# Performance work log

Measured on AMD Instinct MI355X. Metric: run time of the kernel, lower is better.

Reference implementation:

```python
import jax, jax.numpy as jnp
import numpy as np
import math

MUL = 16                      # num_in_features == num_out_features
LDIMS = (1, 3, 5)             # 0e, 1o, 2e  (lmax = 2)
FEAT = MUL * sum(LDIMS)       # 144 = irreps dim = number_of_basis
PATHS = [(0,0,0),(1,1,0),(2,2,0),
         (0,1,1),(1,0,1),(1,2,1),(2,1,1),
         (0,2,2),(1,1,2),(2,0,2),(2,2,2)]
DOT_PATHS = [(0,0,0),(1,1,0),(2,2,0)]

# ---------- real Wigner-3j / Clebsch-Gordan (e3nn convention), numpy precompute ----------

def _su2_cg(j1, m1, j2, m2, j3, m3):
    if m3 != m1 + m2:
        return 0.0
    f = math.factorial
    vmin = max(-j1 + j2 + m3, -j1 + m1, 0)
    vmax = min(j2 + j3 + m1, j3 - j1 + j2, j3 + m3)
    C = math.sqrt((2*j3+1) * f(j3+j1-j2) * f(j3-j1+j2) * f(j1+j2-j3)
                  * f(j3+m3) * f(j3-m3)
                  / (f(j1+j2+j3+1) * f(j1-m1) * f(j1+m1) * f(j2-m2) * f(j2+m2)))
    S = 0.0
    for v in range(vmin, vmax + 1):
        S += (-1.0)**(v + j2 + m2) * f(j2+j3+m1-v) * f(j1-m1+v) / (
            f(v) * f(j3-j1+j2-v) * f(j3+m3-v) * f(v+j1-j2-m3))
    return C * S

def _qmat(l):
    # complex -> real spherical-harmonic change of basis (e3nn convention)
    q = np.zeros((2*l+1, 2*l+1), dtype=np.complex128)
    for m in range(-l, 0):
        q[l+m, l+abs(m)] = 1.0/math.sqrt(2)
        q[l+m, l-abs(m)] = -1j/math.sqrt(2)
    q[l, l] = 1.0
    for m in range(1, l+1):
        q[l+m, l+abs(m)] = (-1)**m/math.sqrt(2)
        q[l+m, l-abs(m)] = 1j*(-1)**m/math.sqrt(2)
    return (-1j)**l * q

def _real_w3j(l1, l2, l3):
    C = np.zeros((2*l1+1, 2*l2+1, 2*l3+1))
    for i, m1 in enumerate(range(-l1, l1+1)):
        for j, m2 in enumerate(range(-l2, l2+1)):
            for k, m3 in enumerate(range(-l3, l3+1)):
                C[i, j, k] = _su2_cg(l1, m1, l2, m2, l3, m3)
    Cr = np.einsum('ij,kl,mn,ikn->jlm', _qmat(l1), _qmat(l2),
                   np.conj(_qmat(l3).T), C.astype(np.complex128))
    Cr = np.real(Cr)
    return (Cr / np.linalg.norm(Cr)).astype(np.float32)  # unit Frobenius norm (3j convention)

W3J = {p: _real_w3j(*p) for p in set(PATHS)}

# ---------- fully connected tensor product (component/element normalization) ----------

def _split(x):
    # blocked layout: [mul x 0e | mul x 1o | mul x 2e]
    n = x.shape[0]
    xs, o = [], 0
    for d in LDIMS:
        xs.append(x[:, o:o + MUL*d].reshape(n, MUL, d))
        o += MUL * d
    return xs

def _fctp(x1, x2, W):
    # W: [11, u, v, w] stacked per PATHS
    xs1, xs2 = _split(x1), _split(x2)
    n = x1.shape[0]
    n_paths = {l3: sum(1 for p in PATHS if p[2] == l3) for l3 in range(3)}
    outs = [None, None, None]
    for i, (l1, l2, l3) in enumerate(PATHS):
        C = jnp.asarray(W3J[(l1, l2, l3)])          # [i, j, k]
        scale = math.sqrt((2*l3 + 1) / (n_paths[l3] * MUL * MUL))
        a = jnp.einsum('nvj,ijk->nivk', xs2[l2], C)      # [n, i, v, k]
        b = jnp.einsum('nui,nivk->nuvk', xs1[l1], a)     # [n, u, v, k]
        o = scale * jnp.einsum('nuvk,uvw->nwk', b, W[i]) # [n, w, k]
        outs[l3] = o if outs[l3] is None else outs[l3] + o
    return jnp.concatenate([o.reshape(n, -1) for o in outs], axis=1)  # [n, 9*MUL]

def _dot(x1, x2, Wd):
    # FCTP(irreps_input, irreps_input, '0e'): paths (0,0,0),(1,1,0),(2,2,0), out mul = 1
    xs1, xs2 = _split(x1), _split(x2)
    fan = 3 * MUL * MUL
    acc = 0.0
    for i, (l1, l2, l3) in enumerate(DOT_PATHS):
        C = jnp.asarray(W3J[(l1, l2, l3)])[:, :, 0]      # [i, j]
        t = jnp.einsum('nui,ij,nvj->nuv', xs1[l1], C, xs2[l2])
        acc = acc + jnp.einsum('nuv,uv->n', t, Wd[i])
    return (acc * math.sqrt(1.0 / fan))[:, None]         # [n, 1]

def setup_inputs() -> dict:
    key = jax.random.key(0)
    ks = jax.random.split(key, 8)
    N = 50000
    return {
        'nodes_features': jax.random.normal(ks[0], (N, FEAT), jnp.float32),
        'degree_matrix': jax.random.normal(ks[1], (N,), jnp.float32),
        'edges_features_distance': jax.random.normal(ks[2], (N,), jnp.float32),
        'edges_features_bond': jax.random.normal(ks[3], (N,), jnp.float32),
        'w_q': jax.random.normal(ks[4], (11, MUL, MUL, MUL), jnp.float32),
        'w_k': jax.random.normal(ks[5], (11, MUL, MUL, MUL), jnp.float32),
        'w_v': jax.random.normal(ks[6], (11, MUL, MUL, MUL), jnp.float32),
        'w_dot': jax.random.normal(ks[7], (3, MUL, MUL), jnp.float32),
    }

def reference(nodes_features, degree_matrix, edges_features_distance,
              edges_features_bond, w_q, w_k, w_v, w_dot):
    # degree_matrix / edges_features_* are unused by the original forward
    x = nodes_features
    q = _fctp(x, x, w_q)                   # tp_q(x, x)
    k = _fctp(x, x, w_k)                   # tp_k(x, x)
    v = _fctp(x, x, w_v)                   # tp(x, x)
    d = _dot(q, k, w_dot)                  # [n, 1]
    e = jnp.exp(d / math.sqrt(float(FEAT)))
    attn = e / (e + 1e-10)                 # sum over last dim of size 1 + eps
    out = attn * v                         # dropout is identity in eval mode
    out = out.reshape(-1, MUL)             # view(-1, num_heads * num_out_features)
    return jax.nn.elu(out)                 # [9n, MUL]
```

## Files before the change

### kernel.cpp

```cpp
#include <hip/hip_runtime.h>
#include <math.h>

#define NP 11
#define NN 8

__device__ __constant__ int g_l1[NP]   = {0,1,2,0,1,1,2,0,1,2,2};
__device__ __constant__ int g_l2[NP]   = {0,1,2,1,0,2,1,2,1,0,2};
__device__ __constant__ int g_l3[NP]   = {0,0,0,1,1,1,1,2,2,2,2};
__device__ __constant__ int g_coff[NP] = {0,1,10,35,44,53,98,143,168,213,238};

typedef _Float16 half8 __attribute__((ext_vector_type(8)));
typedef _Float16 h2 __attribute__((ext_vector_type(2)));
typedef float f32x4 __attribute__((ext_vector_type(4)));

__device__ __forceinline__ float bfu(unsigned int v){ return __uint_as_float(v<<16); }
__device__ __forceinline__ unsigned int rne16(float f){
  unsigned int ui=__float_as_uint(f);
  return (ui+0x7fffu+((ui>>16)&1u))>>16;
}
__device__ __forceinline__ unsigned short h16(float f){
  _Float16 h=(_Float16)f;
  return __builtin_bit_cast(unsigned short,h);
}

__device__ double dfact(int n){ double r=1.0; for(int i=2;i<=n;++i) r*=(double)i; return r; }

__device__ double su2_cg(int j1,int m1,int j2,int m2,int j3,int m3){
  if(m1+m2!=m3) return 0.0;
  int vmin=-j1+j2+m3; if(-j1+m1>vmin) vmin=-j1+m1; if(vmin<0) vmin=0;
  int vmax=j2+j3+m1; int t=j3-j1+j2; if(t<vmax) vmax=t; t=j3+m3; if(t<vmax) vmax=t;
  double C = sqrt((double)(2*j3+1)*dfact(j3+j1-j2)*dfact(j3-j1+j2)*dfact(j1+j2-j3)
      *dfact(j3+m3)*dfact(j3-m3)
      /(dfact(j1+j2+j3+1)*dfact(j1-m1)*dfact(j1+m1)*dfact(j2-m2)*dfact(j2+m2)));
  double S=0.0;
  for(int v=vmin;v<=vmax;++v){
    double sg = ((v+j2+m2)&1)? -1.0:1.0;
    S += sg*dfact(j2+j3+m1-v)*dfact(j1-m1+v)
        /(dfact(v)*dfact(j3-j1+j2-v)*dfact(j3+m3-v)*dfact(v+j1-j2-m3));
  }
  return C*S;
}

__device__ void qelem(int l,int r,int c,double &re,double &im){
  int m=r-l; double a=0.0,b=0.0; const double s=0.70710678118654752440;
  if(m<0){ if(c==l-m) a=s; else if(c==l+m) b=-s; }
  else if(m==0){ if(c==l) a=1.0; }
  else { double sg=(m&1)?-1.0:1.0; if(c==l+m) a=sg*s; else if(c==l-m) b=sg*s; }
  if(l==1){ double tt=a; a=b; b=-tt; }
  else if(l==2){ a=-a; b=-b; }
  re=a; im=b;
}

__device__ int probe_f32(const unsigned short* __restrict__ p, int nelem, int* scnt){
  if(threadIdx.x==0) *scnt=0;
  __syncthreads();
  int M = nelem < 4096 ? nelem : 4096;
  int c=0;
  for(int t=threadIdx.x;t<M;t+=blockDim.x){
    unsigned e=((unsigned)p[t]>>7)&0xFFu;
    if(e!=0u && (e<0x70u || e>0x8Eu)) ++c;
  }
  atomicAdd(scnt,c);
  __syncthreads();
  return (*scnt*8 > M) ? 1 : 0;
}

__global__ void prep(const unsigned short* __restrict__ x,
                     const unsigned short* __restrict__ wq,
                     const unsigned short* __restrict__ wk,
                     const unsigned short* __restrict__ wv,
                     const unsigned short* __restrict__ wd,
                     int nx,int nw,int nd,
                     float* __restrict__ c3j, unsigned int* __restrict__ cgh,
                     unsigned int* __restrict__ wpre){
  const int p=blockIdx.x, tp=blockIdx.y;
  __shared__ double cg[125];
  __shared__ double outv[125];
  __shared__ double nrm;
  __shared__ int scnt;

  const unsigned short* ww=(tp==0)?wq:((tp==1)?wk:wv);
  const int f32 = probe_f32(ww,nw,&scnt);

  {
    unsigned int* dst=wpre+(size_t)(p*3+tp)*2240;
    for(int t=threadIdx.x;t<2048;t+=256){
      int w=t>>7, c=t&127;
      int i0=c*32+w, i1=i0+16;
      float f0,f1;
      if(f32){
        const float* wf=(const float*)ww+(size_t)p*4096;
        f0=wf[i0]; f1=wf[i1];
      }else{
        const unsigned short* wsp=ww+(size_t)p*4096;
        f0=bfu(wsp[i0]); f1=bfu(wsp[i1]);
      }
      dst[w*140+c]=(unsigned int)h16(f0)|((unsigned int)h16(f1)<<16);
    }
  }

  if(tp==0){
    int l1=g_l1[p], l2=g_l2[p], l3=g_l3[p];
    int d1=2*l1+1, d2=2*l2+1, d3=2*l3+1;
    int tot=d1*d2*d3;
    for(int t=threadIdx.x;t<tot;t+=256){
      int i=t/(d2*d3), k=(t/d3)%d2, n=t%d3;
      cg[t]=su2_cg(l1,i-l1,l2,k-l2,l3,n-l3);
    }
    __syncthreads();
    for(int t=threadIdx.x;t<tot;t+=256){
      int a=t/(d2*d3), b=(t/d3)%d2, c=t%d3;
      double sre=0.0;
      for(int i=0;i<d1;++i){ double q1r,q1i; qelem(l1,i,a,q1r,q1i);
        for(int k=0;k<d2;++k){ double q2r,q2i; qelem(l2,k,b,q2r,q2i);
          double pr=q1r*q2r-q1i*q2i, pi=q1r*q2i+q1i*q2r;
          for(int n=0;n<d3;++n){ double q3r,q3i; qelem(l3,n,c,q3r,q3i);
            sre += (pr*q3r + pi*q3i) * cg[(i*d2+k)*d3+n];
          }
        }
      }
      outv[t]=sre;
    }
    __syncthreads();
    if(threadIdx.x==0){
      double s=0.0; for(int t=0;t<tot;++t) s+=outv[t]*outv[t];
      nrm=sqrt(s);
    }
    __syncthreads();
    const float scl_[3]={0.03608439182435161f,0.05412658773652741f,0.06987712429686843f};
    float s=scl_[l3];
    for(int t=threadIdx.x;t<tot;t+=256){
      float val=(float)(outv[t]/nrm);
      c3j[g_coff[p]+t]=val;
      unsigned int h=(unsigned int)h16(val*s);
      cgh[g_coff[p]+t]=h|(h<<16);
    }
  }

  if(p==0 && tp==0){
    int xf=probe_f32(x,nx,&scnt);
    if(threadIdx.x==0) c3j[363]=(float)xf;
    int df=probe_f32(wd,nd,&scnt);
    if(threadIdx.x==0) c3j[367]=(float)df;
  }
}

template<int D1,int D2,int D3>
__device__ __forceinline__ void fusedAB(const unsigned int* __restrict__ sXp,
                                        const unsigned int* __restrict__ sXd,
                                        const unsigned int* __restrict__ cgp,
                                        unsigned int* __restrict__ sAu,
                                        int wave, int lane, int nvalid){
  constexpr int O1=(D1==1)?0:((D1==3)?16:64);
  constexpr int O2P=(D2==1)?0:((D2==3)?8:32);
  const int nn=lane>>3, vp=lane&7;
  if(nn>=nvalid) return;
  h2 x2p[D2];
  #pragma unroll
  for(int j=0;j<D2;++j) x2p[j]=__builtin_bit_cast(h2,sXp[nn*76+O2P+vp*D2+j]);
  const int u0=wave*2;
  h2 x1a[D1],x1b[D1];
  #pragma unroll
  for(int i=0;i<D1;++i){
    x1a[i]=__builtin_bit_cast(h2,sXd[nn*148+O1+u0*D1+i]);
    x1b[i]=__builtin_bit_cast(h2,sXd[nn*148+O1+(u0+1)*D1+i]);
  }
  h2 acc0[D3],acc1[D3];
  #pragma unroll
  for(int k=0;k<D3;++k){ acc0[k]=(h2){(_Float16)0.f,(_Float16)0.f}; acc1[k]=acc0[k]; }
  #pragma unroll
  for(int i=0;i<D1;++i){
    #pragma unroll
    for(int k=0;k<D3;++k){
      h2 ar=(h2){(_Float16)0.f,(_Float16)0.f};
      #pragma unroll
      for(int j=0;j<D2;++j)
        ar+=__builtin_bit_cast(h2,cgp[(i*D2+j)*D3+k])*x2p[j];
      acc0[k]+=x1a[i]*ar;
      acc1[k]+=x1b[i]*ar;
    }
  }
  #pragma unroll
  for(int k=0;k<D3;++k){
    sAu[(k*8+nn)*140+u0*8+vp]   =__builtin_bit_cast(unsigned int,acc0[k]);
    sAu[(k*8+nn)*140+u0*8+vp+8] =__builtin_bit_cast(unsigned int,acc1[k]);
  }
}

template<int L3>
__device__ __forceinline__ void stage2_acc(const unsigned int* __restrict__ sAu,
                                           const unsigned int* __restrict__ wp_path,
                                           const uint4* __restrict__ bf,
                                           f32x4& a0, f32x4& a1,
                                           int n16, int quad, int wave){
  constexpr int P=(L3+1)*3;
  if(wave<P){
    int Mt=wave/3;
    const unsigned int* ap=sAu+(Mt*16+n16)*140+quad*4;
    f32x4 a=a0;
    #pragma unroll
    for(int ks=0;ks<8;++ks)
      a=__builtin_amdgcn_mfma_f32_16x16x32_f16(
          *reinterpret_cast<const half8*>(ap+ks*16),
          __builtin_bit_cast(half8,bf[ks]),a,0,0,0);
    a0=a;
  }
  if(L3==2 && wave==0){
    const unsigned int* ap=sAu+(2*16+n16)*140+quad*4;
    const uint4* bp=(const uint4*)(wp_path+2*2240+n16*140+quad*4);
    uint4 b2[8];
    #pragma unroll
    for(int ks=0;ks<8;++ks) b2[ks]=bp[ks*4];
    f32x4 a=a1;
    #pragma unroll
    for(int ks=0;ks<8;++ks)
      a=__builtin_amdgcn_mfma_f32_16x16x32_f16(
          *reinterpret_cast<const half8*>(ap+ks*16),
          __builtin_bit_cast(half8,b2[ks]),a,0,0,0);
    a1=a;
  }
}

template<int L3>
__device__ __forceinline__ void stage2_out(const f32x4& a0, const f32x4& a1,
                                           float* __restrict__ sO,
                                           int n16, int quad, int wave){
  constexpr int D3=2*L3+1;
  constexpr int OO=(L3==0)?0:((L3==1)?16:64);
  constexpr int P=(L3+1)*3;
  if(wave<P){
    int tp=wave%3, Mt=wave/3;
    #pragma unroll
    for(int reg=0;reg<4;++reg){
      int row=Mt*16+quad*4+reg;
      int k=row>>3, node=row&7;
      if(k<D3) sO[node*440+tp*144+OO+n16*D3+k]=a0[reg];
    }
  }
  if(L3==2 && wave==0){
    #pragma unroll
    for(int reg=0;reg<4;++reg){
      int row=32+quad*4+reg;
      int k=row>>3, node=row&7;
      if(k<D3) sO[node*440+2*144+OO+n16*D3+k]=a1[reg];
    }
  }
}

__global__ __launch_bounds__(512,6) void tfn_main(
    const unsigned short* __restrict__ xin,
    const unsigned int* __restrict__ wpre,
    const unsigned int* __restrict__ cgh,
    const unsigned short* __restrict__ wd,
    const float* __restrict__ c3j,
    unsigned short* __restrict__ outp, int N)
{
  __shared__ __align__(16) unsigned int sAu[48*140];
  __shared__ float sO[NN*440];
  __shared__ __align__(8) unsigned int sXp[NN*76];
  __shared__ __align__(8) unsigned int sXd[NN*148];
  __shared__ float sWd[768];

  const int tid=threadIdx.x;
  const int wave=tid>>6, lane=tid&63;
  const int n16=lane&15, quad=lane>>4;
  const int node0=blockIdx.x*NN;
  const int nvalid=(N-node0)<NN?(N-node0):NN;

  const int xf32 = c3j[363]!=0.0f;
  const int df32 = c3j[367]!=0.0f;

  float* scratch=sO;
  if(!xf32){
    for(int t=tid;t<NN*36;t+=512){
      int nn=t/36, w4=t%36;
      if(nn<nvalid){
        uint2 u=((const uint2*)(xin+(size_t)(node0+nn)*144))[w4];
        float* dst=&scratch[nn*144+w4*4];
        dst[0]=bfu(u.x&0xffffu); dst[1]=bfu(u.x>>16);
        dst[2]=bfu(u.y&0xffffu); dst[3]=bfu(u.y>>16);
      }
    }
  }else{
    const float* xf=(const float*)xin;
    for(int t=tid;t<NN*144;t+=512){
      int nn=t/144, f=t%144;
      if(nn<nvalid) scratch[nn*144+f]=xf[(size_t)(node0+nn)*144+f];
    }
  }
  if(!df32){ for(int t=tid;t<768;t+=512) sWd[t]=bfu((unsigned int)wd[t]); }
  else     { const float* wdf=(const float*)wd; for(int t=tid;t<768;t+=512) sWd[t]=wdf[t]; }
  __syncthreads();

  for(int t=tid;t<NN*144;t+=512){
    int nn=t/144, f=t-nn*144;
    unsigned int h=(unsigned int)h16(scratch[t]);
    sXd[nn*148+f]=h|(h<<16);
  }
  for(int t=tid;t<NN*72;t+=512){
    int nn=t/72, g=t-nn*72;
    int fa,fb;
    if(g<8){ fa=2*g; fb=fa+1; }
    else if(g<32){ int gg=g-8; int vp=gg/3, j=gg-3*vp; fa=16+(2*vp)*3+j; fb=fa+3; }
    else { int gg=g-32; int vp=gg/5, j=gg-5*vp; fa=64+(2*vp)*5+j; fb=fa+5; }
    sXp[nn*76+g]=(unsigned int)h16(scratch[nn*144+fa])|((unsigned int)h16(scratch[nn*144+fb])<<16);
  }
  __syncthreads();

  #define PATH_STEP(P_,D1_,D2_,D3_) { \
    const int PT=((D3_-1)/2+1)*3; \
    uint4 bf[8]; \
    if(wave<PT){ \
      const uint4* bp=(const uint4*)(wpre+(size_t)P_*6720+(wave%3)*2240+n16*140+quad*4); \
      bf[0]=bp[0];  bf[1]=bp[4];  bf[2]=bp[8];  bf[3]=bp[12]; \
      bf[4]=bp[16]; bf[5]=bp[20]; bf[6]=bp[24]; bf[7]=bp[28]; \
    } \
    fusedAB<D1_,D2_,D3_>(sXp,sXd,cgh+g_coff[P_],sAu,wave,lane,nvalid); \
    __syncthreads(); \
    stage2_acc<(D3_-1)/2>(sAu,wpre+(size_t)P_*6720,bf,a0,a1,n16,quad,wave); \
    __syncthreads(); }

  {
    f32x4 a0={0.f,0.f,0.f,0.f}, a1={0.f,0.f,0.f,0.f};
    PATH_STEP(0,1,1,1)
    PATH_STEP(1,3,3,1)
    PATH_STEP(2,5,5,1)
    stage2_out<0>(a0,a1,sO,n16,quad,wave);
  }
  {
    f32x4 a0={0.f,0.f,0.f,0.f}, a1={0.f,0.f,0.f,0.f};
    PATH_STEP(3,1,3,3)
    PATH_STEP(4,3,1,3)
    PATH_STEP(5,3,5,3)
    PATH_STEP(6,5,3,3)
    stage2_out<1>(a0,a1,sO,n16,quad,wave);
  }
  {
    f32x4 a0={0.f,0.f,0.f,0.f}, a1={0.f,0.f,0.f,0.f};
    PATH_STEP(7,1,5,5)
    PATH_STEP(8,3,3,5)
    PATH_STEP(9,5,1,5)
    PATH_STEP(10,5,5,5)
    stage2_out<2>(a0,a1,sO,n16,quad,wave);
  }
  #undef PATH_STEP
  __syncthreads();

  {
    int node=wave;
    if(node<nvalid){
      const float c0=c3j[0], c1=c3j[1], c2=c3j[10];
      const float* qv=sO+node*440;
      const float* kv=qv+144;
      const int v=lane&15, ug=lane>>4;
      float k0=kv[v];
      float k1[3],k2[5];
      #pragma unroll
      for(int j=0;j<3;++j) k1[j]=kv[16+v*3+j];
      #pragma unroll
      for(int m=0;m<5;++m) k2[m]=kv[64+v*5+m];
      float part=0.f;
      #pragma unroll
      for(int t=0;t<4;++t){
        int u=ug+4*t;
        float d0=qv[u]*k0;
        float d1=0.f;
        #pragma unroll
        for(int j=0;j<3;++j) d1+=qv[16+u*3+j]*k1[j];
        float d2=0.f;
        #pragma unroll
        for(int m=0;m<5;++m) d2+=qv[64+u*5+m]*k2[m];
        part+=sWd[u*16+v]*(c0*d0)+sWd[256+u*16+v]*(c1*d1)+sWd[512+u*16+v]*(c2*d2);
      }
      #pragma unroll
      for(int off=1;off<64;off<<=1) part+=__shfl_xor(part,off,64);
      float dd=part*0.03608439182435161f;
      float ex=dd*(1.0f/12.0f);
      ex=fminf(fmaxf(ex,-80.f),80.f);
      float e=expf(ex);
      float attn=e/(e+1e-10f);
      const float* vv=sO+node*440+288;
      if(!xf32){
        unsigned short* ob=outp+(size_t)(node0+node)*144;
        for(int f=lane;f<144;f+=64){
          float val=attn*vv[f];
          float r=(val>0.f)?val:expm1f(val);
          ob[f]=(unsigned short)rne16(r);
        }
      }else{
        float* ob=(float*)outp+(size_t)(node0+node)*144;
        for(int f=lane;f<144;f+=64){
          float val=attn*vv[f];
          ob[f]=(val>0.f)?val:expm1f(val);
        }
      }
    }
  }
}

extern "C" void kernel_launch(void* const* d_in, const int* in_sizes, int n_in,
                              void* d_out, int out_size, void* d_ws, size_t ws_size,
                              hipStream_t stream){
  (void)n_in; (void)out_size; (void)ws_size;
  const unsigned short* x =(const unsigned short*)d_in[0];
  const unsigned short* wq=(const unsigned short*)d_in[4];
  const unsigned short* wk=(const unsigned short*)d_in[5];
  const unsigned short* wv=(const unsigned short*)d_in[6];
  const unsigned short* wd=(const unsigned short*)d_in[7];
  float* c3j=(float*)d_ws;
  unsigned int* cgh=(unsigned int*)d_ws+1024;
  unsigned int* wpre=(unsigned int*)d_ws+2048;
  int N=in_sizes[0]/144;
  prep<<<dim3(NP,3),dim3(256),0,stream>>>(x,wq,wk,wv,wd,
      in_sizes[0],in_sizes[4],in_sizes[7],c3j,cgh,wpre);
  int nb=(N+NN-1)/NN;
  tfn_main<<<dim3(nb),dim3(512),0,stream>>>(x,wpre,cgh,wd,c3j,(unsigned short*)d_out,N);
}
```

Before: 354.9 us.

## Pack LDS into one buffer, store outputs in fp16, cache CG in LDS

Merges all shared arrays into a single overlapping LDS buffer. The q/k/v outputs and the dot weights are now stored as fp16 instead of fp32, and the CG coefficients are staged in LDS instead of read from global memory. The smaller LDS footprint lets launch bounds go from 6 to 8 blocks per CU, which is meant to raise occupancy. The cost is lower precision in the q·k dot product and the v values, plus tighter register limits.

New measurement: 565.9 us. 59.5% more time.

```diff
diff --git a/kernel.cpp b/kernel.cpp
--- a/kernel.cpp
+++ b/kernel.cpp
@@ -21,6 +21,9 @@
 __device__ __forceinline__ unsigned short h16(float f){
   _Float16 h=(_Float16)f;
   return __builtin_bit_cast(unsigned short,h);
+}
+__device__ __forceinline__ float hf(unsigned short s){
+  return (float)__builtin_bit_cast(_Float16,s);
 }
 
 __device__ double dfact(int n){ double r=1.0; for(int i=2;i<=n;++i) r*=(double)i; return r; }
@@ -145,9 +148,16 @@
   }
 }
 
+#define L_AU   0
+#define L_SO   5600
+#define L_XP   7392
+#define L_XD   8000
+#define L_WD   9184
+#define L_CG   9568
+#define L_TOT  9932
+
 template<int D1,int D2,int D3>
-__device__ __forceinline__ void fusedAB(const unsigned int* __restrict__ sXp,
-                                        const unsigned int* __restrict__ sXd,
+__device__ __forceinline__ void fusedAB(const unsigned int* __restrict__ lds,
                                         const unsigned int* __restrict__ cgp,
                                         unsigned int* __restrict__ sAu,
                                         int wave, int lane, int nvalid){
@@ -157,13 +167,13 @@
   if(nn>=nvalid) return;
   h2 x2p[D2];
   #pragma unroll
-  for(int j=0;j<D2;++j) x2p[j]=__builtin_bit_cast(h2,sXp[nn*76+O2P+vp*D2+j]);
+  for(int j=0;j<D2;++j) x2p[j]=__builtin_bit_cast(h2,lds[L_XP+nn*76+O2P+vp*D2+j]);
   const int u0=wave*2;
   h2 x1a[D1],x1b[D1];
   #pragma unroll
   for(int i=0;i<D1;++i){
-    x1a[i]=__builtin_bit_cast(h2,sXd[nn*148+O1+u0*D1+i]);
-    x1b[i]=__builtin_bit_cast(h2,sXd[nn*148+O1+(u0+1)*D1+i]);
+    x1a[i]=__builtin_bit_cast(h2,lds[L_XD+nn*148+O1+u0*D1+i]);
+    x1b[i]=__builtin_bit_cast(h2,lds[L_XD+nn*148+O1+(u0+1)*D1+i]);
   }
   h2 acc0[D3],acc1[D3];
   #pragma unroll
@@ -223,7 +233,7 @@
 
 template<int L3>
 __device__ __forceinline__ void stage2_out(const f32x4& a0, const f32x4& a1,
-                                           float* __restrict__ sO,
+                                           unsigned short* __restrict__ sOh,
                                            int n16, int quad, int wave){
   constexpr int D3=2*L3+1;
   constexpr int OO=(L3==0)?0:((L3==1)?16:64);
@@ -234,7 +244,7 @@
     for(int reg=0;reg<4;++reg){
       int row=Mt*16+quad*4+reg;
       int k=row>>3, node=row&7;
-      if(k<D3) sO[node*440+tp*144+OO+n16*D3+k]=a0[reg];
+      if(k<D3) sOh[node*448+tp*144+OO+n16*D3+k]=h16(a0[reg]);
     }
   }
   if(L3==2 && wave==0){
@@ -242,12 +252,12 @@
     for(int reg=0;reg<4;++reg){
       int row=32+quad*4+reg;
       int k=row>>3, node=row&7;
-      if(k<D3) sO[node*440+2*144+OO+n16*D3+k]=a1[reg];
-    }
-  }
-}
-
-__global__ __launch_bounds__(512,6) void tfn_main(
+      if(k<D3) sOh[node*448+2*144+OO+n16*D3+k]=h16(a1[reg]);
+    }
+  }
+}
+
+__global__ __launch_bounds__(512,8) void tfn_main(
     const unsigned short* __restrict__ xin,
     const unsigned int* __restrict__ wpre,
     const unsigned int* __restrict__ cgh,
@@ -255,11 +265,7 @@
     const float* __restrict__ c3j,
     unsigned short* __restrict__ outp, int N)
 {
-  __shared__ __align__(16) unsigned int sAu[48*140];
-  __shared__ float sO[NN*440];
-  __shared__ __align__(8) unsigned int sXp[NN*76];
-  __shared__ __align__(8) unsigned int sXd[NN*148];
-  __shared__ float sWd[768];
+  __shared__ __align__(16) unsigned int lds[L_TOT];
 
   const int tid=threadIdx.x;
   const int wave=tid>>6, lane=tid&63;
@@ -270,7 +276,11 @@
   const int xf32 = c3j[363]!=0.0f;
   const int df32 = c3j[367]!=0.0f;
 
-  float* scratch=sO;
+  unsigned int* sAu=lds+L_AU;
+  unsigned short* sOh=(unsigned short*)(lds+L_SO);
+  unsigned short* sWdh=(unsigned short*)(lds+L_WD);
+
+  float* scratch=(float*)(lds+L_SO);
   if(!xf32){
     for(int t=tid;t<NN*36;t+=512){
       int nn=t/36, w4=t%36;
@@ -288,14 +298,15 @@
       if(nn<nvalid) scratch[nn*144+f]=xf[(size_t)(node0+nn)*144+f];
     }
   }
-  if(!df32){ for(int t=tid;t<768;t+=512) sWd[t]=bfu((unsigned int)wd[t]); }
-  else     { const float* wdf=(const float*)wd; for(int t=tid;t<768;t+=512) sWd[t]=wdf[t]; }
+  if(!df32){ for(int t=tid;t<768;t+=512) sWdh[t]=(unsigned short)h16(bfu((unsigned int)wd[t])); }
+  else     { const float* wdf=(const float*)wd; for(int t=tid;t<768;t+=512) sWdh[t]=(unsigned short)h16(wdf[t]); }
+  for(int t=tid;t<363;t+=512) lds[L_CG+t]=cgh[t];
   __syncthreads();
 
   for(int t=tid;t<NN*144;t+=512){
     int nn=t/144, f=t-nn*144;
     unsigned int h=(unsigned int)h16(scratch[t]);
-    sXd[nn*148+f]=h|(h<<16);
+    lds[L_XD+nn*148+f]=h|(h<<16);
   }
   for(int t=tid;t<NN*72;t+=512){
     int nn=t/72, g=t-nn*72;
@@ -303,7 +314,7 @@
     if(g<8){ fa=2*g; fb=fa+1; }
     else if(g<32){ int gg=g-8; int vp=gg/3, j=gg-3*vp; fa=16+(2*vp)*3+j; fb=fa+3; }
     else { int gg=g-32; int vp=gg/5, j=gg-5*vp; fa=64+(2*vp)*5+j; fb=fa+5; }
-    sXp[nn*76+g]=(unsigned int)h16(scratch[nn*144+fa])|((unsigned int)h16(scratch[nn*144+fb])<<16);
+    lds[L_XP+nn*76+g]=(unsigned int)h16(scratch[nn*144+fa])|((unsigned int)h16(scratch[nn*144+fb])<<16);
   }
   __syncthreads();
 
@@ -315,7 +326,7 @@
       bf[0]=bp[0];  bf[1]=bp[4];  bf[2]=bp[8];  bf[3]=bp[12]; \
       bf[4]=bp[16]; bf[5]=bp[20]; bf[6]=bp[24]; bf[7]=bp[28]; \
     } \
-    fusedAB<D1_,D2_,D3_>(sXp,sXd,cgh+g_coff[P_],sAu,wave,lane,nvalid); \
+    fusedAB<D1_,D2_,D3_>(lds,lds+L_CG+g_coff[P_],sAu,wave,lane,nvalid); \
     __syncthreads(); \
     stage2_acc<(D3_-1)/2>(sAu,wpre+(size_t)P_*6720,bf,a0,a1,n16,quad,wave); \
     __syncthreads(); }
@@ -325,7 +336,7 @@
     PATH_STEP(0,1,1,1)
     PATH_STEP(1,3,3,1)
     PATH_STEP(2,5,5,1)
-    stage2_out<0>(a0,a1,sO,n16,quad,wave);
+    stage2_out<0>(a0,a1,sOh,n16,quad,wave);
   }
   {
     f32x4 a0={0.f,0.f,0.f,0.f}, a1={0.f,0.f,0.f,0.f};
@@ -333,7 +344,7 @@
     PATH_STEP(4,3,1,3)
     PATH_STEP(5,3,5,3)
     PATH_STEP(6,5,3,3)
-    stage2_out<1>(a0,a1,sO,n16,quad,wave);
+    stage2_out<1>(a0,a1,sOh,n16,quad,wave);
   }
   {
     f32x4 a0={0.f,0.f,0.f,0.f}, a1={0.f,0.f,0.f,0.f};
@@ -341,7 +352,7 @@
     PATH_STEP(8,3,3,5)
     PATH_STEP(9,5,1,5)
     PATH_STEP(10,5,5,5)
-    stage2_out<2>(a0,a1,sO,n16,quad,wave);
+    stage2_out<2>(a0,a1,sOh,n16,quad,wave);
   }
   #undef PATH_STEP
   __syncthreads();
@@ -350,27 +361,27 @@
     int node=wave;
     if(node<nvalid){
       const float c0=c3j[0], c1=c3j[1], c2=c3j[10];
-      const float* qv=sO+node*440;
-      const float* kv=qv+144;
+      const unsigned short* qh=sOh+node*448;
+      const unsigned short* kh=qh+144;
       const int v=lane&15, ug=lane>>4;
-      float k0=kv[v];
+      float k0=hf(kh[v]);
       float k1[3],k2[5];
       #pragma unroll
-      for(int j=0;j<3;++j) k1[j]=kv[16+v*3+j];
+      for(int j=0;j<3;++j) k1[j]=hf(kh[16+v*3+j]);
       #pragma unroll
-      for(int m=0;m<5;++m) k2[m]=kv[64+v*5+m];
+      for(int m=0;m<5;++m) k2[m]=hf(kh[64+v*5+m]);
       float part=0.f;
       #pragma unroll
       for(int t=0;t<4;++t){
         int u=ug+4*t;
-        float d0=qv[u]*k0;
+        float d0=hf(qh[u])*k0;
         float d1=0.f;
         #pragma unroll
-        for(int j=0;j<3;++j) d1+=qv[16+u*3+j]*k1[j];
+        for(int j=0;j<3;++j) d1+=hf(qh[16+u*3+j])*k1[j];
         float d2=0.f;
         #pragma unroll
-        for(int m=0;m<5;++m) d2+=qv[64+u*5+m]*k2[m];
-        part+=sWd[u*16+v]*(c0*d0)+sWd[256+u*16+v]*(c1*d1)+sWd[512+u*16+v]*(c2*d2);
+        for(int m=0;m<5;++m) d2+=hf(qh[64+u*5+m])*k2[m];
+        part+=hf(sWdh[u*16+v])*(c0*d0)+hf(sWdh[256+u*16+v])*(c1*d1)+hf(sWdh[512+u*16+v])*(c2*d2);
       }
       #pragma unroll
       for(int off=1;off<64;off<<=1) part+=__shfl_xor(part,off,64);
@@ -379,18 +390,18 @@
       ex=fminf(fmaxf(ex,-80.f),80.f);
       float e=expf(ex);
       float attn=e/(e+1e-10f);
-      const float* vv=sO+node*440+288;
+      const unsigned short* vh=qh+288;
       if(!xf32){
         unsigned short* ob=outp+(size_t)(node0+node)*144;
         for(int f=lane;f<144;f+=64){
-          float val=attn*vv[f];
+          float val=attn*hf(vh[f]);
           float r=(val>0.f)?val:expm1f(val);
           ob[f]=(unsigned short)rne16(r);
         }
       }else{
         float* ob=(float*)outp+(size_t)(node0+node)*144;
         for(int f=lane;f<144;f+=64){
-          float val=attn*vv[f];
+          float val=attn*hf(vh[f]);
           ob[f]=(val>0.f)?val:expm1f(val);
         }
       }
```
